# Performance work log

Hardware: AMD Instinct MI355X
Metric: run time of the kernel (lower is better)

## Reference

```python
import jax, jax.numpy as jnp
import numpy as np

B, S, D, H, WS = 2, 4096, 768, 12, 256
HD = D // H
NW = S // WS
EPS = 1e-5


def layernorm(x, g, b):
    mu = jnp.mean(x, axis=-1, keepdims=True)
    var = jnp.mean(jnp.square(x - mu), axis=-1, keepdims=True)
    return (x - mu) * jax.lax.rsqrt(var + EPS) * g + b


def setup_inputs() -> dict:
    key = jax.random.key(0)
    ks = jax.random.split(key, 8)
    s = 0.02
    return {
        "x": jax.random.normal(ks[0], (B, S, D), dtype=jnp.float32),
        "Wq": jax.random.normal(ks[1], (D, D), dtype=jnp.float32) * s,
        "bq": jnp.zeros((D,), jnp.float32),
        "Wk": jax.random.normal(ks[2], (D, D), dtype=jnp.float32) * s,
        "bk": jnp.zeros((D,), jnp.float32),
        "Wv": jax.random.normal(ks[3], (D, D), dtype=jnp.float32) * s,
        "bv": jnp.zeros((D,), jnp.float32),
        "Wo": jax.random.normal(ks[4], (D, D), dtype=jnp.float32) * s,
        "bo": jnp.zeros((D,), jnp.float32),
        "ln1_g": jnp.ones((D,), jnp.float32),
        "ln1_b": jnp.zeros((D,), jnp.float32),
        "W1": jax.random.normal(ks[5], (D, 4 * D), dtype=jnp.float32) * s,
        "b1": jnp.zeros((4 * D,), jnp.float32),
        "W2": jax.random.normal(ks[6], (4 * D, D), dtype=jnp.float32) * s,
        "b2": jnp.zeros((D,), jnp.float32),
        "ln2_g": jnp.ones((D,), jnp.float32),
        "ln2_b": jnp.zeros((D,), jnp.float32),
    }


def _attn(h, Wq, bq, Wk, bk, Wv, bv, Wo, bo):
    q = (h @ Wq + bq).reshape(B, S, H, HD)
    k = (h @ Wk + bk).reshape(B, S, H, HD)
    v = (h @ Wv + bv).reshape(B, S, H, HD)
    # split into windows: [B, NW, WS, H, HD]
    kb = k.reshape(B, NW, WS, H, HD)
    vb = v.reshape(B, NW, WS, H, HD)
    qw = jnp.moveaxis(q.reshape(B, NW, WS, H, HD), 1, 0)  # [NW, B, WS, H, HD]
    inv = 1.0 / np.sqrt(HD).astype(np.float32)

    def step(carry, qi_i):
        qi, i = qi_i  # qi: [B, WS, H, HD]
        # per key-window scores: [B, H, NW, WSq, WSk]
        scores = jnp.einsum('bqhd,bjkhd->bhjqk', qi, kb) * inv
        attn = jax.nn.softmax(scores, axis=-1)  # per-block softmax (as in source)
        mask = (jnp.arange(NW) <= i).astype(attn.dtype)  # block-causal, include own window
        attn = attn * mask[None, None, :, None, None]
        ctx = jnp.einsum('bhjqk,bjkhd->bqhd', attn, vb)  # sum over key windows
        return carry, ctx

    _, ctxs = jax.lax.scan(step, None, (qw, jnp.arange(NW)))
    ctx = jnp.moveaxis(ctxs, 0, 1).reshape(B, S, D)
    return ctx @ Wo + bo


def reference(x, Wq, bq, Wk, bk, Wv, bv, Wo, bo, ln1_g, ln1_b, W1, b1, W2, b2, ln2_g, ln2_b):
    attn_out = _attn(layernorm(x, ln1_g, ln1_b), Wq, bq, Wk, bk, Wv, bv, Wo, bo)
    x = x + attn_out
    h2 = layernorm(x, ln2_g, ln2_b)
    ff = jax.nn.gelu(h2 @ W1 + b1, approximate=False) @ W2 + b2
    return x + ff
```

## Files before the change

### kernel.cpp

```cpp
#include <hip/hip_runtime.h>
#include <cstdint>
#include <cstddef>

#define DEV __device__ __forceinline__

typedef unsigned short u16;
typedef unsigned int u32;
typedef __attribute__((ext_vector_type(8))) short s16x8;
typedef __attribute__((ext_vector_type(4))) float f32x4;

typedef unsigned int u32_as1 __attribute__((address_space(1)));
typedef unsigned int u32_as3 __attribute__((address_space(3)));

DEV u16 f2bf(float f){
  unsigned u = __float_as_uint(f);
  u += 0x7fffu + ((u >> 16) & 1u);
  return (u16)(u >> 16);
}

DEV u32 cvtpk_bf16(float lo, float hi){
  u32 r;
  asm("v_cvt_pk_bf16_f32 %0, %1, %2" : "=v"(r) : "v"(lo), "v"(hi));
  return r;
}

DEV void gload16(const void* g, void* l){
  __builtin_amdgcn_global_load_lds((const u32_as1*)g, (u32_as3*)l, 16, 0, 0);
}

template<int NZ>
__global__ __launch_bounds__(256) void wconv_kernel(
    const float* __restrict__ Wa, const float* __restrict__ Wb,
    const float* __restrict__ Wc, const float* __restrict__ Wd,
    u16* __restrict__ Da, u16* __restrict__ Db, u16* __restrict__ Dc, u16* __restrict__ Dd,
    int K, int N){
  __shared__ float tl[32][33];
  int z = (NZ>1) ? blockIdx.z : 0;
  const float* W = (z==0)?Wa:(z==1)?Wb:(z==2)?Wc:Wd;
  u16* Wt = (z==0)?Da:(z==1)?Db:(z==2)?Dc:Dd;
  int tx = threadIdx.x & 31, ty = threadIdx.x >> 5;
  int k0 = blockIdx.x * 32, n0 = blockIdx.y * 32;
  #pragma unroll
  for (int p=0;p<4;p++)
    tl[ty+8*p][tx] = W[(size_t)(k0+ty+8*p)*N + (n0+tx)];
  __syncthreads();
  #pragma unroll
  for (int p=0;p<4;p++){
    int n = ty+8*p;
    Wt[(size_t)(n0+n)*K + (k0+tx)] = f2bf(tl[tx][n]);
  }
}

__global__ __launch_bounds__(256) void vconv_kernel(const u16* __restrict__ vbuf,
                                                    u16* __restrict__ vtb){
  __shared__ u16 TL[64][65];
  int t = threadIdx.x;
  int kt = blockIdx.x, bh = blockIdx.y;
  int b = bh / 12, h = bh - b*12;
  const u16* src = vbuf + ((size_t)(b*4096 + kt*64) * 768) + h*64;
  int d = t & 63, kg = t >> 6;
  #pragma unroll
  for (int j=0;j<16;j++){
    int k = kg*16 + j;
    TL[k][d] = src[(size_t)k*768 + d];
  }
  __syncthreads();
  u16* dst = vtb + ((size_t)bh*64)*4096 + (size_t)kt*64;
  #pragma unroll
  for (int it=0; it<2; it++){
    int idx = it*256 + t;
    int dd = idx >> 3, gn = idx & 7;
    s16x8 o;
    #pragma unroll
    for (int e=0;e<8;e++){
      int klocal = (gn>>2)*32 + 4*(gn&3) + (e>>1) + 16*(e&1);
      ((u16*)&o)[e] = TL[klocal][dd];
    }
    *(s16x8*)(dst + (size_t)dd*4096 + gn*8) = o;
  }
}

__global__ __launch_bounds__(256) void ln_kernel(const float* __restrict__ x,
                                                 const float* __restrict__ g,
                                                 const float* __restrict__ bta,
                                                 u16* __restrict__ out){
  int row = blockIdx.x, t = threadIdx.x;
  const float* xr = x + (size_t)row*768;
  float v0 = xr[t], v1 = xr[t+256], v2 = xr[t+512];
  float s = v0+v1+v2, s2 = v0*v0+v1*v1+v2*v2;
  #pragma unroll
  for (int m=1;m<64;m<<=1){ s += __shfl_xor(s,m); s2 += __shfl_xor(s2,m); }
  __shared__ float ls[4], ls2[4];
  int w = t>>6;
  if ((t&63)==0){ ls[w]=s; ls2[w]=s2; }
  __syncthreads();
  s = ls[0]+ls[1]+ls[2]+ls[3]; s2 = ls2[0]+ls2[1]+ls2[2]+ls2[3];
  float mu = s*(1.0f/768.0f);
  float rstd = rsqrtf(s2*(1.0f/768.0f) - mu*mu + 1e-5f);
  u16* orow = out + (size_t)row*768;
  orow[t]     = f2bf((v0-mu)*rstd*g[t]     + bta[t]);
  orow[t+256] = f2bf((v1-mu)*rstd*g[t+256] + bta[t+256]);
  orow[t+512] = f2bf((v2-mu)*rstd*g[t+512] + bta[t+512]);
}

template<bool GELU, bool RES, bool OUTBF16, int BM>
__global__ __launch_bounds__(256) void gemm_kernel(
    const u16* __restrict__ A, const u16* __restrict__ Bt0, size_t btStride,
    const float* __restrict__ bias0, const float* __restrict__ bias1, const float* __restrict__ bias2,
    const float* __restrict__ res, void* __restrict__ out0, size_t outStride,
    int M, int N, int K, float qscale)
{
  constexpr int AM = BM/32;
  __shared__ u16 As[BM*64];
  __shared__ u16 Bs[128*64];
  const int t = threadIdx.x, lane = t & 63, w = t >> 6;
  const int lj = lane & 15, g = lane >> 4;
  const int wm = w >> 1, wn = w & 1;
  const int z = blockIdx.z;
  const u16* Bt = Bt0 + (size_t)z * btStride;
  const float* bias = (z==0) ? bias0 : (z==1 ? bias1 : bias2);
  const u16* Arow = A  + (size_t)blockIdx.x * BM * K;
  const u16* Brow = Bt + (size_t)blockIdx.y * 128 * K;

  f32x4 acc[AM][4];
  #pragma unroll
  for (int a=0;a<AM;a++)
    #pragma unroll
    for (int b=0;b<4;b++){ f32x4 zz = {0.f,0.f,0.f,0.f}; acc[a][b] = zz; }

  for (int kk=0; kk<K; kk+=64){
    #pragma unroll
    for (int cc=0;cc<BM/32;cc++){
      int c = cc*256 + t;
      int row = c>>3, gp = c&7;
      gload16(Arow + (size_t)row*K + kk + ((gp ^ (row&7))<<3),
              (void*)(As + (size_t)(cc*256 + w*64)*8));
    }
    #pragma unroll
    for (int cc=0;cc<4;cc++){
      int c = cc*256 + t;
      int row = c>>3, gp = c&7;
      gload16(Brow + (size_t)row*K + kk + ((gp ^ (row&7))<<3),
              (void*)(Bs + (size_t)(cc*256 + w*64)*8));
    }
    __syncthreads();
    #pragma unroll
    for (int ks=0;ks<2;ks++){
      s16x8 af[AM], bfr[4];
      #pragma unroll
      for (int mt=0;mt<AM;mt++){
        int row = wm*(BM/2)+mt*16+lj;
        af[mt]  = *(const s16x8*)&As[(size_t)row*64 + (((ks*4+g) ^ (lj&7))<<3)];
      }
      #pragma unroll
      for (int nt=0;nt<4;nt++){
        int row = wn*64+nt*16+lj;
        bfr[nt] = *(const s16x8*)&Bs[(size_t)row*64 + (((ks*4+g) ^ (lj&7))<<3)];
      }
      #pragma unroll
      for (int mt=0;mt<AM;mt++)
        #pragma unroll
        for (int nt=0;nt<4;nt++)
          acc[mt][nt] = __builtin_amdgcn_mfma_f32_16x16x32_bf16(af[mt], bfr[nt], acc[mt][nt], 0,0,0);
    }
    __syncthreads();
  }

  const size_t gr0 = (size_t)blockIdx.x*BM + wm*(BM/2);
  const int gc0 = blockIdx.y*128 + wn*64;
  float* outF = (float*)out0; u16* outB = (u16*)out0;
  if (OUTBF16) outB += (size_t)z*outStride; else outF += (size_t)z*outStride;
  #pragma unroll
  for (int mt=0;mt<AM;mt++)
    #pragma unroll
    for (int nt=0;nt<4;nt++){
      int gc = gc0 + nt*16 + lj;
      float bv = bias[gc];
      #pragma unroll
      for (int r=0;r<4;r++){
        size_t gr = gr0 + mt*16 + g*4 + r;
        float val = acc[mt][nt][r] + bv;
        if (z==0) val *= qscale;
        if (RES)  val += res[gr*(size_t)N + gc];
        if (GELU) val = 0.5f*val*(1.0f + erff(val*0.70710678118f));
        if (OUTBF16) outB[gr*(size_t)N + gc] = f2bf(val);
        else         outF[gr*(size_t)N + gc] = val;
      }
    }
}

__global__ __launch_bounds__(256,3) void attn_kernel(
    const u16* __restrict__ qb, const u16* __restrict__ kb,
    const u16* __restrict__ vtb, u16* __restrict__ ctx)
{
  __shared__ u16 KV[256*64];
  __shared__ u32 Ps[4][16*20];
  const int t = threadIdx.x, lane = t & 63, w = t >> 6;
  const int lj = lane & 15, g = lane >> 4;
  const int bx = blockIdx.x;
  const int pp = bx & 7, qq = (bx >> 3) & 3, bh = bx >> 5;
  const int h = bh % 12, b = bh / 12;
  const size_t seqbase = (size_t)b * 4096;
  const int hoff = h * 64;

  #pragma unroll
  for (int f=0; f<2; f++){
    const int iw = f ? (15 - pp) : pp;
    const int qrow0 = iw*256 + qq*64 + w*16;

    s16x8 qa[2];
    #pragma unroll
    for (int ks=0;ks<2;ks++)
      qa[ks] = *(const s16x8*)(qb + (seqbase + qrow0 + lj)*768 + hoff + ks*32 + g*8);

    f32x4 cacc[4];
    #pragma unroll
    for (int dt=0;dt<4;dt++){ f32x4 zz = {0.f,0.f,0.f,0.f}; cacc[dt] = zz; }

    for (int jw=0; jw<=iw; jw++){
      const u16* kwin = kb + (seqbase + jw*256)*768 + hoff;
      const u16* vtwin = vtb + (size_t)bh*64*4096 + jw*256;

      __syncthreads();
      #pragma unroll
      for (int cc=0;cc<8;cc++){
        int c = cc*256 + t;
        int krow = c>>3, vp = c&7;
        gload16(kwin + (size_t)krow*768 + ((vp ^ (krow&7))<<3),
                (void*)(KV + (size_t)(cc*256 + w*64)*8));
      }
      __syncthreads();

      f32x4 sacc[16];
      #pragma unroll
      for (int kt=0;kt<16;kt++){ f32x4 zz = {0.f,0.f,0.f,0.f}; sacc[kt] = zz; }
      __builtin_amdgcn_s_setprio(1);
      #pragma unroll
      for (int kt=0;kt<16;kt++){
        int kl = kt*16 + lj;
        #pragma unroll
        for (int ks=0;ks<2;ks++){
          s16x8 kf = *(const s16x8*)&KV[ (size_t)kl*64 + (((4*ks+g) ^ (kl&7))<<3) ];
          sacc[kt] = __builtin_amdgcn_mfma_f32_16x16x32_bf16(qa[ks], kf, sacc[kt], 0,0,0);
        }
      }
      __builtin_amdgcn_s_setprio(0);
      __syncthreads();

      #pragma unroll
      for (int cc=0;cc<8;cc++){
        int c = cc*256 + t;
        int d = c>>5, cp = c&31;
        gload16(vtwin + (size_t)d*4096 + ((cp ^ (d&15))<<3),
                (void*)(KV + (size_t)(cc*256 + w*64)*8));
      }

      float sm[4], rs[4];
      #pragma unroll
      for (int r=0;r<4;r++) sm[r] = 0.f;
      #pragma unroll
      for (int kt=0;kt<16;kt++)
        #pragma unroll
        for (int r=0;r<4;r++){
          float pv = exp2f(sacc[kt][r]);
          sacc[kt][r] = pv; sm[r] += pv;
        }
      #pragma unroll
      for (int msk=1; msk<16; msk<<=1)
        #pragma unroll
        for (int r=0;r<4;r++) sm[r] += __shfl_xor(sm[r], msk);
      #pragma unroll
      for (int r=0;r<4;r++) rs[r] = 1.0f / sm[r];

      __syncthreads();

      f32x4 pacc[4];
      #pragma unroll
      for (int dt=0;dt<4;dt++){ f32x4 zz = {0.f,0.f,0.f,0.f}; pacc[dt] = zz; }
      #pragma unroll
      for (int ks=0;ks<8;ks++){
        #pragma unroll
        for (int r=0;r<4;r++)
          Ps[w][ (4*g+r)*20 + lj ] = cvtpk_bf16(sacc[2*ks][r], sacc[2*ks+1][r]);
        s16x8 pa = *(const s16x8*)&Ps[w][ lj*20 + g*4 ];
        __builtin_amdgcn_s_setprio(1);
        #pragma unroll
        for (int dt=0;dt<4;dt++){
          int d = dt*16 + lj;
          s16x8 vf = *(const s16x8*)&KV[ (size_t)d*256 + (((4*ks+g) ^ (d&15))<<3) ];
          pacc[dt] = __builtin_amdgcn_mfma_f32_16x16x32_bf16(pa, vf, pacc[dt], 0,0,0);
        }
        __builtin_amdgcn_s_setprio(0);
      }
      #pragma unroll
      for (int dt=0;dt<4;dt++)
        #pragma unroll
        for (int r=0;r<4;r++)
          cacc[dt][r] += rs[r] * pacc[dt][r];
    }

    #pragma unroll
    for (int dt=0;dt<4;dt++)
      #pragma unroll
      for (int r=0;r<4;r++){
        int qrow = qrow0 + g*4 + r;
        ctx[ (seqbase + qrow)*768 + hoff + dt*16 + lj ] = f2bf(cacc[dt][r]);
      }
  }
}

extern "C" void kernel_launch(void* const* d_in, const int* in_sizes, int n_in,
                              void* d_out, int out_size, void* d_ws, size_t ws_size,
                              hipStream_t stream)
{
  const float* x    = (const float*)d_in[0];
  const float* Wq   = (const float*)d_in[1];
  const float* bq   = (const float*)d_in[2];
  const float* Wk   = (const float*)d_in[3];
  const float* bk   = (const float*)d_in[4];
  const float* Wv   = (const float*)d_in[5];
  const float* bv   = (const float*)d_in[6];
  const float* Wo   = (const float*)d_in[7];
  const float* bo   = (const float*)d_in[8];
  const float* ln1g = (const float*)d_in[9];
  const float* ln1b = (const float*)d_in[10];
  const float* W1   = (const float*)d_in[11];
  const float* b1   = (const float*)d_in[12];
  const float* W2   = (const float*)d_in[13];
  const float* b2   = (const float*)d_in[14];
  const float* ln2g = (const float*)d_in[15];
  const float* ln2b = (const float*)d_in[16];

  char* ws = (char*)d_ws;
  constexpr size_t SZ_W768  = (size_t)768*768*2;
  constexpr size_t SZ_W3072 = (size_t)768*3072*2;
  constexpr size_t SZ_HB    = (size_t)8192*768*2;
  u16* wtq = (u16*)(ws);
  u16* wtk = (u16*)(ws + SZ_W768);
  u16* wtv = (u16*)(ws + 2*SZ_W768);
  u16* wto = (u16*)(ws + 3*SZ_W768);
  u16* wt1 = (u16*)(ws + 4*SZ_W768);
  u16* wt2 = (u16*)(ws + 4*SZ_W768 + SZ_W3072);
  char* p0 = ws + 4*SZ_W768 + 2*SZ_W3072;
  u16*   hbuf = (u16*)p0;
  u16*   qbuf = (u16*)(p0 + SZ_HB);
  u16*   kbuf = (u16*)(p0 + 2*SZ_HB);
  u16*   vbuf = (u16*)(p0 + 3*SZ_HB);
  u16*   cbuf = (u16*)(p0 + 4*SZ_HB);
  float* x1   = (float*)(p0 + 5*SZ_HB);
  u16*   vtbuf = hbuf;
  u16*   ffa  = qbuf;
  float* outp = (float*)d_out;

  wconv_kernel<4><<<dim3(24,24,4), 256, 0, stream>>>(
      Wq, Wk, Wv, Wo, wtq, wtk, wtv, wto, 768, 768);
  wconv_kernel<1><<<dim3(24,96), 256, 0, stream>>>(
      W1, W1, W1, W1, wt1, wt1, wt1, wt1, 768, 3072);
  wconv_kernel<1><<<dim3(96,24), 256, 0, stream>>>(
      W2, W2, W2, W2, wt2, wt2, wt2, wt2, 3072, 768);

  ln_kernel<<<8192, 256, 0, stream>>>(x, ln1g, ln1b, hbuf);
  gemm_kernel<false,false,true,128><<<dim3(64,6,3), 256, 0, stream>>>(
      hbuf, wtq, (size_t)768*768, bq, bk, bv, nullptr, qbuf, (size_t)8192*768,
      8192, 768, 768, 0.180336880111f);
  vconv_kernel<<<dim3(64,24), 256, 0, stream>>>(vbuf, vtbuf);
  attn_kernel<<<768, 256, 0, stream>>>(qbuf, kbuf, vtbuf, cbuf);
  gemm_kernel<false,true,false,64><<<dim3(128,6,1), 256, 0, stream>>>(
      cbuf, wto, 0, bo, bo, bo, x, x1, 0, 8192, 768, 768, 1.0f);
  ln_kernel<<<8192, 256, 0, stream>>>(x1, ln2g, ln2b, hbuf);
  gemm_kernel<true,false,true,128><<<dim3(64,24,1), 256, 0, stream>>>(
      hbuf, wt1, 0, b1, b1, b1, nullptr, ffa, 0, 8192, 3072, 768, 1.0f);
  gemm_kernel<false,true,false,64><<<dim3(128,6,1), 256, 0, stream>>>(
      ffa, wt2, 0, b2, b2, b2, x1, outp, 0, 8192, 768, 3072, 1.0f);
}
```

Before: 324.0 us.

## Transpose QK^T MFMA to keep P in registers and skip LDS round-trip

Swaps the MFMA operand order for the score computation so each lane holds a row of scores. The P tile can then be packed straight into the A operand of the PV MFMA, with no staging through shared memory. The row sum now needs only two cross-lane shuffles, normalisation is folded into P before accumulating directly into cacc, and hardware v_exp/v_rcp are used. The change also raises attention occupancy to 4 blocks per SM and shrinks the QKV GEMM tile to 64 rows with twice the grid. Normalising P before the bf16 rounding and using the approximate rcp/exp may shift numerics slightly.

```diff
diff --git a/kernel.cpp b/kernel.cpp
--- a/kernel.cpp
+++ b/kernel.cpp
@@ -8,6 +8,7 @@
 typedef unsigned int u32;
 typedef __attribute__((ext_vector_type(8))) short s16x8;
 typedef __attribute__((ext_vector_type(4))) float f32x4;
+typedef __attribute__((ext_vector_type(4))) unsigned int u32x4;
 
 typedef unsigned int u32_as1 __attribute__((address_space(1)));
 typedef unsigned int u32_as3 __attribute__((address_space(3)));
@@ -21,6 +22,18 @@
 DEV u32 cvtpk_bf16(float lo, float hi){
   u32 r;
   asm("v_cvt_pk_bf16_f32 %0, %1, %2" : "=v"(r) : "v"(lo), "v"(hi));
+  return r;
+}
+
+DEV float fexp2(float x){
+  float r;
+  asm("v_exp_f32 %0, %1" : "=v"(r) : "v"(x));
+  return r;
+}
+
+DEV float frcp(float x){
+  float r;
+  asm("v_rcp_f32 %0, %1" : "=v"(r) : "v"(x));
   return r;
 }
 
@@ -189,12 +202,11 @@
     }
 }
 
-__global__ __launch_bounds__(256,3) void attn_kernel(
+__global__ __launch_bounds__(256,4) void attn_kernel(
     const u16* __restrict__ qb, const u16* __restrict__ kb,
     const u16* __restrict__ vtb, u16* __restrict__ ctx)
 {
   __shared__ u16 KV[256*64];
-  __shared__ u32 Ps[4][16*20];
   const int t = threadIdx.x, lane = t & 63, w = t >> 6;
   const int lj = lane & 15, g = lane >> 4;
   const int bx = blockIdx.x;
@@ -241,7 +253,7 @@
         #pragma unroll
         for (int ks=0;ks<2;ks++){
           s16x8 kf = *(const s16x8*)&KV[ (size_t)kl*64 + (((4*ks+g) ^ (kl&7))<<3) ];
-          sacc[kt] = __builtin_amdgcn_mfma_f32_16x16x32_bf16(qa[ks], kf, sacc[kt], 0,0,0);
+          sacc[kt] = __builtin_amdgcn_mfma_f32_16x16x32_bf16(kf, qa[ks], sacc[kt], 0,0,0);
         }
       }
       __builtin_amdgcn_s_setprio(0);
@@ -255,48 +267,36 @@
                 (void*)(KV + (size_t)(cc*256 + w*64)*8));
       }
 
-      float sm[4], rs[4];
-      #pragma unroll
-      for (int r=0;r<4;r++) sm[r] = 0.f;
+      float sm = 0.f;
       #pragma unroll
       for (int kt=0;kt<16;kt++)
         #pragma unroll
         for (int r=0;r<4;r++){
-          float pv = exp2f(sacc[kt][r]);
-          sacc[kt][r] = pv; sm[r] += pv;
+          float pv = fexp2(sacc[kt][r]);
+          sacc[kt][r] = pv; sm += pv;
         }
-      #pragma unroll
-      for (int msk=1; msk<16; msk<<=1)
-        #pragma unroll
-        for (int r=0;r<4;r++) sm[r] += __shfl_xor(sm[r], msk);
-      #pragma unroll
-      for (int r=0;r<4;r++) rs[r] = 1.0f / sm[r];
+      sm += __shfl_xor(sm, 16);
+      sm += __shfl_xor(sm, 32);
+      float rs = frcp(sm);
 
       __syncthreads();
 
-      f32x4 pacc[4];
-      #pragma unroll
-      for (int dt=0;dt<4;dt++){ f32x4 zz = {0.f,0.f,0.f,0.f}; pacc[dt] = zz; }
       #pragma unroll
       for (int ks=0;ks<8;ks++){
+        u32x4 pw;
         #pragma unroll
         for (int r=0;r<4;r++)
-          Ps[w][ (4*g+r)*20 + lj ] = cvtpk_bf16(sacc[2*ks][r], sacc[2*ks+1][r]);
-        s16x8 pa = *(const s16x8*)&Ps[w][ lj*20 + g*4 ];
+          pw[r] = cvtpk_bf16(sacc[2*ks][r]*rs, sacc[2*ks+1][r]*rs);
+        s16x8 pa = __builtin_bit_cast(s16x8, pw);
         __builtin_amdgcn_s_setprio(1);
         #pragma unroll
         for (int dt=0;dt<4;dt++){
           int d = dt*16 + lj;
           s16x8 vf = *(const s16x8*)&KV[ (size_t)d*256 + (((4*ks+g) ^ (d&15))<<3) ];
-          pacc[dt] = __builtin_amdgcn_mfma_f32_16x16x32_bf16(pa, vf, pacc[dt], 0,0,0);
+          cacc[dt] = __builtin_amdgcn_mfma_f32_16x16x32_bf16(pa, vf, cacc[dt], 0,0,0);
         }
         __builtin_amdgcn_s_setprio(0);
       }
-      #pragma unroll
-      for (int dt=0;dt<4;dt++)
-        #pragma unroll
-        for (int r=0;r<4;r++)
-          cacc[dt][r] += rs[r] * pacc[dt][r];
     }
 
     #pragma unroll
@@ -360,7 +360,7 @@
       W2, W2, W2, W2, wt2, wt2, wt2, wt2, 3072, 768);
 
   ln_kernel<<<8192, 256, 0, stream>>>(x, ln1g, ln1b, hbuf);
-  gemm_kernel<false,false,true,128><<<dim3(64,6,3), 256, 0, stream>>>(
+  gemm_kernel<false,false,true,64><<<dim3(128,6,3), 256, 0, stream>>>(
       hbuf, wtq, (size_t)768*768, bq, bk, bv, nullptr, qbuf, (size_t)8192*768,
       8192, 768, 768, 0.180336880111f);
   vconv_kernel<<<dim3(64,24), 256, 0, stream>>>(vbuf, vtbuf);
```

Measured after the change: 326.5 us. Within noise of the previous version (+0.8%).
